# Performance work log

Measured on AMD Instinct MI355X. Metric: run time of the kernel, lower is better.

The kernel has to match this reference:

```python
import jax, jax.numpy as jnp
import numpy as np

NB = 16   # num_blocks
DIN = 64  # per-block input dim
DOUT = 64 # per-block output dim
NT = 2    # n_templates (ns)


def setup_inputs() -> dict:
    key = jax.random.key(0)
    k1, k2, k3, k4, k5 = jax.random.split(key, 5)
    T, B = 2048, 8
    a = 0.1  # GroupLinearLayer init range
    x = jax.random.normal(k1, (T, B, NB * DIN), dtype=jnp.float32)
    module_emb = 0.1 * jax.random.normal(k2, (1, 1, NB * DIN), dtype=jnp.float32)
    read_w = jax.random.uniform(k3, (1, DIN, NT), dtype=jnp.float32, minval=-a, maxval=a)
    lim = 1.0 / np.sqrt(DIN)  # nn.Linear default init range
    w_stack = jax.random.uniform(k4, (NT, DOUT, DIN), dtype=jnp.float32, minval=-lim, maxval=lim)
    b_stack = jax.random.uniform(k5, (NT, DOUT), dtype=jnp.float32, minval=-lim, maxval=lim)
    return {"x": x, "module_emb": module_emb, "read_w": read_w,
            "w_stack": w_stack, "b_stack": b_stack}


def reference(x, module_emb, read_w, w_stack, b_stack):
    T, B, D = x.shape
    # add module embedding (broadcast over T, B)
    new_x = x + module_emb
    # flatten to per-block tokens: (N, DIN) with N = T*B*NB
    xf = new_x.reshape(T * B * NB, DIN)
    # routing logits via GroupLinearLayer with 1 block: (N, NT)
    logits = xf @ read_w[0]
    att = jax.nn.softmax(logits, axis=-1)
    # apply each template Linear: (N, NT, DOUT)
    x_next = jnp.einsum('nd,tod->nto', xf, w_stack) + b_stack[None, :, :]
    # soft combine templates; mean over singleton dim is identity
    out = jnp.einsum('nt,nto->no', att, x_next)
    return out.reshape(T, B, NB * DOUT)
```

## Files before the change

### kernel.cpp

```cpp
#include <hip/hip_runtime.h>


#define NBLK 1024
#define TPW  4

typedef short bf16x8 __attribute__((ext_vector_type(8)));
typedef float f32x4  __attribute__((ext_vector_type(4)));

union B8 { bf16x8 v; unsigned u[4]; };

__device__ __forceinline__ unsigned pk2bf(float lo, float hi) {
    unsigned a = __float_as_uint(lo) + 0x8000u;
    unsigned b = __float_as_uint(hi) + 0x8000u;
    return __builtin_amdgcn_perm(b, a, 0x07060302u);
}

__device__ __forceinline__ void pack8(B8& d, float4 p, float4 q) {
    d.u[0] = pk2bf(p.x, p.y); d.u[1] = pk2bf(p.z, p.w);
    d.u[2] = pk2bf(q.x, q.y); d.u[3] = pk2bf(q.z, q.w);
}

__global__ __launch_bounds__(256, 3) void sgll_kernel(
    const float* __restrict__ x,
    const float* __restrict__ emb,
    const float* __restrict__ rw,
    const float* __restrict__ ws,
    const float* __restrict__ bs,
    float* __restrict__ out)
{
    __shared__ bf16x8 sW1[8][64];
    __shared__ bf16x8 sWd[8][64];

    const int tid  = threadIdx.x;
    const int lane = tid & 63;
    const int wv   = tid >> 6;
    const int col  = lane & 15;
    const int q    = lane >> 4;

    #pragma unroll
    for (int c = wv; c < 8; c += 4) {
        const int kt = c >> 2, ot = c & 3;
        const float* p0 = ws + (ot * 16 + col) * 64 + kt * 32 + q * 8;
        const float* p1 = p0 + 4096;
        float4 a0 = *(const float4*)p0, a1 = *(const float4*)(p0 + 4);
        float4 c0 = *(const float4*)p1, c1 = *(const float4*)(p1 + 4);
        B8 f1, fd;
        pack8(f1, c0, c1);
        fd.u[0] = pk2bf(a0.x - c0.x, a0.y - c0.y);
        fd.u[1] = pk2bf(a0.z - c0.z, a0.w - c0.w);
        fd.u[2] = pk2bf(a1.x - c1.x, a1.y - c1.y);
        fd.u[3] = pk2bf(a1.z - c1.z, a1.w - c1.w);
        sW1[c][lane] = f1.v;
        sWd[c][lane] = fd.v;
    }

    B8 R0, R1;
    {
        const int c01 = col & 1;
        float v[8];
        #pragma unroll
        for (int j = 0; j < 8; ++j)
            v[j] = rw[(q * 8 + j) * 2 + c01];
        pack8(R0, make_float4(v[0], v[1], v[2], v[3]), make_float4(v[4], v[5], v[6], v[7]));
        #pragma unroll
        for (int j = 0; j < 8; ++j)
            v[j] = rw[(32 + q * 8 + j) * 2 + c01];
        pack8(R1, make_float4(v[0], v[1], v[2], v[3]), make_float4(v[4], v[5], v[6], v[7]));
    }

    B8 E0, E1;
    {
        const float* ep = emb + col * 64 + q * 8;
        pack8(E0, *(const float4*)ep, *(const float4*)(ep + 4));
        pack8(E1, *(const float4*)(ep + 32), *(const float4*)(ep + 36));
    }
    f32x4 bI1[4], bId[4];
    #pragma unroll
    for (int ot = 0; ot < 4; ++ot) {
        float4 b1 = *(const float4*)(bs + 64 + ot * 16 + q * 4);
        float4 b0 = *(const float4*)(bs + ot * 16 + q * 4);
        bI1[ot][0] = b1.x; bI1[ot][1] = b1.y; bI1[ot][2] = b1.z; bI1[ot][3] = b1.w;
        bId[ot][0] = b0.x - b1.x; bId[ot][1] = b0.y - b1.y;
        bId[ot][2] = b0.z - b1.z; bId[ot][3] = b0.w - b1.w;
    }

    __syncthreads();

    const long base = (long)(blockIdx.x * 4 + wv) * (TPW * 16);
    float4 buf[TPW][4];
    #pragma unroll
    for (int t = 0; t < TPW; ++t) {
        const float* p = x + (base + (long)t * 16 + col) * 64 + q * 8;
        buf[t][0] = *(const float4*)p;        buf[t][1] = *(const float4*)(p + 4);
        buf[t][2] = *(const float4*)(p + 32); buf[t][3] = *(const float4*)(p + 36);
    }
    __builtin_amdgcn_sched_barrier(0);

    f32x4 I1[4], Id[4], Il;
    #pragma unroll
    for (int ot = 0; ot < 4; ++ot) {
        f32x4 a1 = bI1[ot], ad = bId[ot];
        a1 = __builtin_amdgcn_mfma_f32_16x16x32_bf16(sW1[ot][lane],     E0.v, a1, 0, 0, 0);
        a1 = __builtin_amdgcn_mfma_f32_16x16x32_bf16(sW1[4 + ot][lane], E1.v, a1, 0, 0, 0);
        ad = __builtin_amdgcn_mfma_f32_16x16x32_bf16(sWd[ot][lane],     E0.v, ad, 0, 0, 0);
        ad = __builtin_amdgcn_mfma_f32_16x16x32_bf16(sWd[4 + ot][lane], E1.v, ad, 0, 0, 0);
        I1[ot] = a1;
        Id[ot] = ad;
    }
    {
        f32x4 z = {0.f, 0.f, 0.f, 0.f};
        z = __builtin_amdgcn_mfma_f32_16x16x32_bf16(R0.v, E0.v, z, 0, 0, 0);
        z = __builtin_amdgcn_mfma_f32_16x16x32_bf16(R1.v, E1.v, z, 0, 0, 0);
        Il = z;
    }

    #pragma unroll
    for (int i = 0; i < TPW; ++i) {
        B8 X0, X1;
        pack8(X0, buf[i][0], buf[i][1]);
        pack8(X1, buf[i][2], buf[i][3]);

        f32x4 lac = Il;
        lac = __builtin_amdgcn_mfma_f32_16x16x32_bf16(R0.v, X0.v, lac, 0, 0, 0);
        lac = __builtin_amdgcn_mfma_f32_16x16x32_bf16(R1.v, X1.v, lac, 0, 0, 0);
        const float att = 1.0f / (1.0f + __expf(lac[1] - lac[0]));

        const long rowoff = (base + (long)i * 16 + col) * 64;
        #pragma unroll
        for (int ot = 0; ot < 4; ++ot) {
            f32x4 y = I1[ot];
            y = __builtin_amdgcn_mfma_f32_16x16x32_bf16(sW1[ot][lane],     X0.v, y, 0, 0, 0);
            y = __builtin_amdgcn_mfma_f32_16x16x32_bf16(sW1[4 + ot][lane], X1.v, y, 0, 0, 0);
            f32x4 d = Id[ot];
            d = __builtin_amdgcn_mfma_f32_16x16x32_bf16(sWd[ot][lane],     X0.v, d, 0, 0, 0);
            d = __builtin_amdgcn_mfma_f32_16x16x32_bf16(sWd[4 + ot][lane], X1.v, d, 0, 0, 0);
            f32x4 o;
            o[0] = fmaf(att, d[0], y[0]);
            o[1] = fmaf(att, d[1], y[1]);
            o[2] = fmaf(att, d[2], y[2]);
            o[3] = fmaf(att, d[3], y[3]);
            __builtin_nontemporal_store(o, (f32x4*)(out + rowoff + ot * 16 + q * 4));
        }
    }
}

extern "C" void kernel_launch(void* const* d_in, const int* in_sizes, int n_in,
                              void* d_out, int out_size, void* d_ws, size_t ws_size,
                              hipStream_t stream) {
    const float* x   = (const float*)d_in[0];
    const float* emb = (const float*)d_in[1];
    const float* rw  = (const float*)d_in[2];
    const float* wsk = (const float*)d_in[3];
    const float* bs  = (const float*)d_in[4];
    float* out = (float*)d_out;
    sgll_kernel<<<NBLK, 256, 0, stream>>>(x, emb, rw, wsk, bs, out);
}
```

Baseline: 140.8 us.

## Use persistent 768-block grid with strided tiles and register double-buffered prefetch

Shrinks the grid from 1024 to 768 blocks. Each wave now handles 5 or 6 tiles strided by the total wave count instead of 4 contiguous tiles. Four tile buffers are loaded up front, and two are refilled with later tiles right after packing, so global loads overlap MFMA compute. Output stores switch from nontemporal to normal stores. This aims to spread work evenly across CUs and hide memory latency, at the cost of uneven per-wave tile counts and extra register pressure.

```diff
diff --git a/kernel.cpp b/kernel.cpp
--- a/kernel.cpp
+++ b/kernel.cpp
@@ -1,8 +1,9 @@
 #include <hip/hip_runtime.h>
 
 
-#define NBLK 1024
-#define TPW  4
+#define NBLK   768
+#define WAVES  (NBLK * 4)
+#define NTILES 16384
 
 typedef short bf16x8 __attribute__((ext_vector_type(8)));
 typedef float f32x4  __attribute__((ext_vector_type(4)));
@@ -86,14 +87,19 @@
 
     __syncthreads();
 
-    const long base = (long)(blockIdx.x * 4 + wv) * (TPW * 16);
-    float4 buf[TPW][4];
-    #pragma unroll
-    for (int t = 0; t < TPW; ++t) {
-        const float* p = x + (base + (long)t * 16 + col) * 64 + q * 8;
-        buf[t][0] = *(const float4*)p;        buf[t][1] = *(const float4*)(p + 4);
-        buf[t][2] = *(const float4*)(p + 32); buf[t][3] = *(const float4*)(p + 36);
-    }
+    const int w = blockIdx.x * 4 + wv;
+
+    auto loadt = [&](float4 (&B)[4], int T) {
+        const float* p = x + ((long)T * 16 + col) * 64 + q * 8;
+        B[0] = *(const float4*)p;        B[1] = *(const float4*)(p + 4);
+        B[2] = *(const float4*)(p + 32); B[3] = *(const float4*)(p + 36);
+    };
+
+    float4 bA[4], bB[4], bC[4], bD[4];
+    loadt(bA, w);
+    loadt(bB, w + WAVES);
+    loadt(bC, w + 2 * WAVES);
+    loadt(bD, w + 3 * WAVES);
     __builtin_amdgcn_sched_barrier(0);
 
     f32x4 I1[4], Id[4], Il;
@@ -114,18 +120,18 @@
         Il = z;
     }
 
-    #pragma unroll
-    for (int i = 0; i < TPW; ++i) {
+    auto step = [&](float4 (&B)[4], int TI, bool refill, int RT) {
         B8 X0, X1;
-        pack8(X0, buf[i][0], buf[i][1]);
-        pack8(X1, buf[i][2], buf[i][3]);
+        pack8(X0, B[0], B[1]);
+        pack8(X1, B[2], B[3]);
+        if (refill) loadt(B, RT);
 
         f32x4 lac = Il;
         lac = __builtin_amdgcn_mfma_f32_16x16x32_bf16(R0.v, X0.v, lac, 0, 0, 0);
         lac = __builtin_amdgcn_mfma_f32_16x16x32_bf16(R1.v, X1.v, lac, 0, 0, 0);
         const float att = 1.0f / (1.0f + __expf(lac[1] - lac[0]));
 
-        const long rowoff = (base + (long)i * 16 + col) * 64;
+        const long rowoff = ((long)TI * 16 + col) * 64;
         #pragma unroll
         for (int ot = 0; ot < 4; ++ot) {
             f32x4 y = I1[ot];
@@ -134,14 +140,24 @@
             f32x4 d = Id[ot];
             d = __builtin_amdgcn_mfma_f32_16x16x32_bf16(sWd[ot][lane],     X0.v, d, 0, 0, 0);
             d = __builtin_amdgcn_mfma_f32_16x16x32_bf16(sWd[4 + ot][lane], X1.v, d, 0, 0, 0);
-            f32x4 o;
-            o[0] = fmaf(att, d[0], y[0]);
-            o[1] = fmaf(att, d[1], y[1]);
-            o[2] = fmaf(att, d[2], y[2]);
-            o[3] = fmaf(att, d[3], y[3]);
-            __builtin_nontemporal_store(o, (f32x4*)(out + rowoff + ot * 16 + q * 4));
+            float4 o;
+            o.x = fmaf(att, d[0], y[0]);
+            o.y = fmaf(att, d[1], y[1]);
+            o.z = fmaf(att, d[2], y[2]);
+            o.w = fmaf(att, d[3], y[3]);
+            *(float4*)(out + rowoff + ot * 16 + q * 4) = o;
         }
-    }
+    };
+
+    const bool six = (w < NTILES - 5 * WAVES);
+
+    step(bA, w,             true, w + 4 * WAVES);
+    step(bB, w +     WAVES, six,  w + 5 * WAVES);
+    step(bC, w + 2 * WAVES, false, 0);
+    step(bD, w + 3 * WAVES, false, 0);
+    step(bA, w + 4 * WAVES, false, 0);
+    if (six)
+        step(bB, w + 5 * WAVES, false, 0);
 }
 
 extern "C" void kernel_launch(void* const* d_in, const int* in_sizes, int n_in,
```

Result: faster. 137.5 us (-2.4%).

## Stream x tiles through an LDS ring with async global_load_lds

Applied to the files above, without the earlier changes.

Replaces the register-held prefetch of all x tiles with a per-wave 4-deep ring buffer in LDS, filled by global_load_lds DMA, and drains it with manual vmcnt waits and swizzled ds_read_b128 reads. Each wave now handles 8 tiles over half as many blocks, and occupancy drops to 2 blocks per CU. Outputs are buffered in registers and written at the end with regular stores instead of nontemporal ones. The aim is to overlap HBM loads with MFMA work and keep more bytes in flight. In exchange it uses 64KB of LDS per block, raises register pressure from the outs array, and depends on hand-counted waitcnt values being correct.

```diff
diff --git a/kernel.cpp b/kernel.cpp
--- a/kernel.cpp
+++ b/kernel.cpp
@@ -1,8 +1,9 @@
 #include <hip/hip_runtime.h>
 
 
-#define NBLK 1024
-#define TPW  4
+#define NBLK 512
+#define TPW  8
+#define DEPTH 4
 
 typedef short bf16x8 __attribute__((ext_vector_type(8)));
 typedef float f32x4  __attribute__((ext_vector_type(4)));
@@ -20,7 +21,12 @@
     d.u[2] = pk2bf(q.x, q.y); d.u[3] = pk2bf(q.z, q.w);
 }
 
-__global__ __launch_bounds__(256, 3) void sgll_kernel(
+__device__ __forceinline__ void pack8v(B8& d, f32x4 p, f32x4 r) {
+    d.u[0] = pk2bf(p[0], p[1]); d.u[1] = pk2bf(p[2], p[3]);
+    d.u[2] = pk2bf(r[0], r[1]); d.u[3] = pk2bf(r[2], r[3]);
+}
+
+__global__ __launch_bounds__(256, 2) void sgll_kernel(
     const float* __restrict__ x,
     const float* __restrict__ emb,
     const float* __restrict__ rw,
@@ -30,6 +36,7 @@
 {
     __shared__ bf16x8 sW1[8][64];
     __shared__ bf16x8 sWd[8][64];
+    __shared__ float  sX[4][DEPTH * 1024];
 
     const int tid  = threadIdx.x;
     const int lane = tid & 63;
@@ -86,15 +93,28 @@
 
     __syncthreads();
 
-    const long base = (long)(blockIdx.x * 4 + wv) * (TPW * 16);
-    float4 buf[TPW][4];
-    #pragma unroll
-    for (int t = 0; t < TPW; ++t) {
-        const float* p = x + (base + (long)t * 16 + col) * 64 + q * 8;
-        buf[t][0] = *(const float4*)p;        buf[t][1] = *(const float4*)(p + 4);
-        buf[t][2] = *(const float4*)(p + 32); buf[t][3] = *(const float4*)(p + 36);
-    }
-    __builtin_amdgcn_sched_barrier(0);
+    const int w = blockIdx.x * 4 + wv;
+    const long base = (long)w * (TPW * 16);
+    const float* const xb = x + base * 64;
+    float* const ring = &sX[wv][0];
+
+    const unsigned ldsb = (unsigned)(uintptr_t)ring;
+    const unsigned C0 = ldsb + col * 256 + (((2 * q + 0) ^ col) << 4);
+    const unsigned C1 = ldsb + col * 256 + (((2 * q + 1) ^ col) << 4);
+    const unsigned C2 = ldsb + col * 256 + (((8 + 2 * q + 0) ^ col) << 4);
+    const unsigned C3 = ldsb + col * 256 + (((8 + 2 * q + 1) ^ col) << 4);
+
+    auto dma = [&](int T, int slot) {
+        #pragma unroll
+        for (int k = 0; k < 4; ++k) {
+            const int tk = k * 4 + q;
+            const float* g = xb + T * 1024 + tk * 64 + ((col ^ tk) << 2);
+            __builtin_amdgcn_global_load_lds(g, ring + slot * 1024 + k * 256, 16, 0, 0);
+        }
+    };
+
+    #pragma unroll
+    for (int t = 0; t < DEPTH; ++t) dma(t, t);
 
     f32x4 I1[4], Id[4], Il;
     #pragma unroll
@@ -114,18 +134,34 @@
         Il = z;
     }
 
+    f32x4 outs[TPW][4];
+
     #pragma unroll
     for (int i = 0; i < TPW; ++i) {
+        if (i <= 4)      asm volatile("s_waitcnt vmcnt(12)");
+        else if (i == 5) asm volatile("s_waitcnt vmcnt(8)");
+        else if (i == 6) asm volatile("s_waitcnt vmcnt(4)");
+        else             asm volatile("s_waitcnt vmcnt(0)");
+
+        f32x4 r0, r1, r2, r3;
+        asm volatile("ds_read_b128 %0, %1 offset:%c2" : "=v"(r0) : "v"(C0), "i"((i & 3) * 4096));
+        asm volatile("ds_read_b128 %0, %1 offset:%c2" : "=v"(r1) : "v"(C1), "i"((i & 3) * 4096));
+        asm volatile("ds_read_b128 %0, %1 offset:%c2" : "=v"(r2) : "v"(C2), "i"((i & 3) * 4096));
+        asm volatile("ds_read_b128 %0, %1 offset:%c2" : "=v"(r3) : "v"(C3), "i"((i & 3) * 4096));
+        asm volatile("s_waitcnt lgkmcnt(0)");
+        __builtin_amdgcn_sched_barrier(0);
+
+        if (i + DEPTH < TPW) dma(i + DEPTH, i & 3);
+
         B8 X0, X1;
-        pack8(X0, buf[i][0], buf[i][1]);
-        pack8(X1, buf[i][2], buf[i][3]);
+        pack8v(X0, r0, r1);
+        pack8v(X1, r2, r3);
 
         f32x4 lac = Il;
         lac = __builtin_amdgcn_mfma_f32_16x16x32_bf16(R0.v, X0.v, lac, 0, 0, 0);
         lac = __builtin_amdgcn_mfma_f32_16x16x32_bf16(R1.v, X1.v, lac, 0, 0, 0);
         const float att = 1.0f / (1.0f + __expf(lac[1] - lac[0]));
 
-        const long rowoff = (base + (long)i * 16 + col) * 64;
         #pragma unroll
         for (int ot = 0; ot < 4; ++ot) {
             f32x4 y = I1[ot];
@@ -139,8 +175,16 @@
             o[1] = fmaf(att, d[1], y[1]);
             o[2] = fmaf(att, d[2], y[2]);
             o[3] = fmaf(att, d[3], y[3]);
-            __builtin_nontemporal_store(o, (f32x4*)(out + rowoff + ot * 16 + q * 4));
+            outs[i][ot] = o;
         }
+    }
+
+    #pragma unroll
+    for (int i = 0; i < TPW; ++i) {
+        const long rowoff = (base + (long)i * 16 + col) * 64;
+        #pragma unroll
+        for (int ot = 0; ot < 4; ++ot)
+            *(f32x4*)(out + rowoff + ot * 16 + q * 4) = outs[i][ot];
     }
 }
 
```

Measured after the change: 136.2 us. -3.3%, faster.
